# Optimization experiments

Measured on AMD Instinct MI355X. Metric: run time of the kernel, lower is better.

## Reference

```python
import math
import jax, jax.numpy as jnp
import numpy as np

D_MODEL = 1024
NUM_HEADS = 16
HEAD_DIM = D_MODEL // NUM_HEADS
EPS = 1e-8


def setup_inputs() -> dict:
    key = jax.random.key(0)
    ks = jax.random.split(key, 9)
    B, T = 2, 2048
    scale = 1.0 / math.sqrt(D_MODEL)
    return {
        "query": jax.random.normal(ks[0], (B, T, D_MODEL), jnp.float32),
        "key": jax.random.normal(ks[1], (B, T, D_MODEL), jnp.float32),
        "value": jax.random.normal(ks[2], (B, T, D_MODEL), jnp.float32),
        "key_padding_mask": jnp.zeros((B, T), dtype=bool),
        "Wq": jax.random.normal(ks[3], (D_MODEL, D_MODEL), jnp.float32) * scale,
        "Wk": jax.random.normal(ks[4], (D_MODEL, D_MODEL), jnp.float32) * scale,
        "Wv": jax.random.normal(ks[5], (D_MODEL, D_MODEL), jnp.float32) * scale,
        "Wo": jax.random.normal(ks[6], (D_MODEL, D_MODEL), jnp.float32) * scale,
        "s_v": jnp.zeros((NUM_HEADS,), jnp.float32),
        "s_r": jnp.zeros((NUM_HEADS,), jnp.float32),
    }


def _l2norm(x, eps=EPS):
    n = jnp.sqrt(jnp.sum(x * x, axis=-1, keepdims=True))
    return x / jnp.maximum(n, eps)


def _tanh_norm(x, eps=EPS):
    # Reconstructed TanhNorm: bound each head vector by tanh of its L2 norm.
    n = jnp.sqrt(jnp.sum(x * x, axis=-1, keepdims=True))
    return jnp.tanh(n) * x / (n + eps)


def reference(query, key, value, key_padding_mask, Wq, Wk, Wv, Wo, s_v, s_r):
    B, T_q, _ = query.shape
    T_k = key.shape[1]
    H, D = NUM_HEADS, HEAD_DIM

    def proj_split(x, W):  # torch Linear: x @ W.T, then split heads -> (B,H,T,D)
        y = jnp.einsum('btm,dm->btd', x, W)
        return y.reshape(x.shape[0], x.shape[1], H, D).transpose(0, 2, 1, 3)

    q = _l2norm(proj_split(query, Wq))
    k = _l2norm(proj_split(key, Wk))
    v = _l2norm(proj_split(value, Wv))

    sim = jnp.einsum('bhqd,bhkd->bhqk', q, k)  # cosine similarities

    w = jnp.exp(s_v) + 1.0  # (H,) window size per head
    r = jnp.exp(s_r) + 1.0  # (H,) sharpness per head

    # Trim-and-Square: alpha = relu(1 - r*(1 - sim))^2
    alpha = jax.nn.relu(1.0 - r[None, :, None, None] * (1.0 - sim)) ** 2

    # Causal cosine softmask: (H, T_q, T_k)
    rel = (jnp.arange(T_k)[None, :] - jnp.arange(T_q)[:, None]).astype(jnp.float32)
    w_ = w[:, None, None]
    cos_mask = 0.5 * (jnp.cos(jnp.pi * rel[None] / w_) + 1.0)
    in_window = (rel[None] > -w_) & (rel[None] <= 0)
    softmask = cos_mask * in_window.astype(jnp.float32)
    alpha = alpha * softmask[None]

    alpha = jnp.where(key_padding_mask[:, None, None, :], 0.0, alpha)

    out = jnp.einsum('bhqk,bhkd->bhqd', alpha, v)
    out = _tanh_norm(out)
    out = out.transpose(0, 2, 1, 3).reshape(B, T_q, H * D)
    return jnp.einsum('btm,dm->btd', out, Wo)
```

## Files before the change

kernel.cpp:

```cpp
#include <hip/hip_runtime.h>
#include <math.h>

#define D_MODEL 1024
#define NUM_HEADS 16
#define HEAD_DIM 64
#define EPS 1e-8f
#define B_SZ 2
#define T_SZ 2048
#define KEXP 2048

typedef unsigned short ushort_t;
typedef __attribute__((ext_vector_type(8))) short bf16x8;
typedef __attribute__((ext_vector_type(4))) float f32x4;

__device__ __forceinline__ ushort_t f2bf(float f) {
    unsigned u = __float_as_uint(f);
    unsigned r = (u + 0x7FFFu + ((u >> 16) & 1u)) >> 16;
    return (ushort_t)r;
}
__device__ __forceinline__ float bf2f(ushort_t h) {
    return __uint_as_float(((unsigned)h) << 16);
}

__device__ __forceinline__ void gload_lds16(const ushort_t* g, ushort_t* l) {
    __builtin_amdgcn_global_load_lds(
        (const __attribute__((address_space(1))) unsigned int*)g,
        (__attribute__((address_space(3))) unsigned int*)l, 16, 0, 0);
}

__global__ __launch_bounds__(256) void expand7(
    const float* q, const float* k, const float* v,
    const float* wq, const float* wk, const float* wv, const float* wo,
    ushort_t* qe, ushort_t* ke, ushort_t* ve,
    ushort_t* wqe, ushort_t* wke, ushort_t* wve, ushort_t* woe)
{
    const float* in; ushort_t* out; int rows;
    switch (blockIdx.z) {
        case 0: in = q;  out = qe;  rows = 4096; break;
        case 1: in = k;  out = ke;  rows = 4096; break;
        case 2: in = v;  out = ve;  rows = 4096; break;
        case 3: in = wq; out = wqe; rows = 1024; break;
        case 4: in = wk; out = wke; rows = 1024; break;
        case 5: in = wv; out = wve; rows = 1024; break;
        default: in = wo; out = woe; rows = 1024; break;
    }
    const int gid = blockIdx.x * 256 + threadIdx.x;
    const int total = rows * 1024;
    for (int e = gid * 8; e < total; e += 1024 * 256 * 8) {
        const int row = e >> 10;
        const int kk = e & 1023;

        float x[8];
        *(float4*)&x[0] = *(const float4*)&in[(size_t)row * 1024 + kk];
        *(float4*)&x[4] = *(const float4*)&in[(size_t)row * 1024 + kk + 4];

        union { ushort_t s[8]; uint4 u; } hi, lo;
        #pragma unroll
        for (int i = 0; i < 8; ++i) {
            ushort_t h = f2bf(x[i]);
            hi.s[i] = h;
            lo.s[i] = f2bf(x[i] - bf2f(h));
        }
        ushort_t* dst = out + (size_t)row * KEXP + (kk >> 5) * 64 + (kk & 31);
        *(uint4*)dst        = hi.u;
        *(uint4*)(dst + 32) = lo.u;
    }
}

__global__ __launch_bounds__(256) void gemm_sb3(
    const ushort_t* A0, const ushort_t* B0, float* C0,
    const ushort_t* A1, const ushort_t* B1, float* C1,
    const ushort_t* A2, const ushort_t* B2, float* C2,
    int M, int N)
{
    constexpr int BM = 128, BN = 128, WAVES_N = 2;
    constexpr int WAVE_M = 64, WAVE_N = 64, FM = 4, FN = 4;

    const int gx = gridDim.x, gy = gridDim.y;
    const int nwg = gx * gy * gridDim.z;
    const int lid = blockIdx.x + gx * (blockIdx.y + gy * blockIdx.z);
    const int cpx = nwg >> 3;
    const int swz = (lid & 7) * cpx + (lid >> 3);
    const int bz  = swz / (gx * gy);
    const int rem = swz - bz * gx * gy;
    const int by  = rem / gx;
    const int bx  = rem - by * gx;

    const ushort_t* Ae; const ushort_t* Be; float* C;
    if (bz == 0)      { Ae = A0; Be = B0; C = C0; }
    else if (bz == 1) { Ae = A1; Be = B1; C = C1; }
    else              { Ae = A2; Be = B2; C = C2; }

    __shared__ __align__(16) ushort_t As[BM * 64];
    __shared__ __align__(16) ushort_t Bs[BN * 64];

    const int tid = threadIdx.x;
    const int bm = by * BM;
    const int bn = bx * BN;

    const int rr = tid >> 3;
    const int p  = tid & 7;

    const int wid  = tid >> 6;
    const int wm   = wid / WAVES_N;
    const int wn   = wid % WAVES_N;
    const int lane = tid & 63;
    const int lrow = lane & 15;
    const int lk   = lane >> 4;

    f32x4 acc[FM][FN] = {};

    for (int ks = 0; ks < 32; ++ks) {
        const int kb = ks * 64;
        #pragma unroll
        for (int r = 0; r < 4; ++r) {
            const int row = r * 32 + rr;
            const int s = p ^ (row & 7);
            gload_lds16(Ae + (size_t)(bm + row) * KEXP + kb + s * 8,
                        &As[row * 64 + p * 8]);
        }
        #pragma unroll
        for (int r = 0; r < 4; ++r) {
            const int row = r * 32 + rr;
            const int s = p ^ (row & 7);
            gload_lds16(Be + (size_t)(bn + row) * KEXP + kb + s * 8,
                        &Bs[row * 64 + p * 8]);
        }
        __syncthreads();

        bf16x8 ah[FM], al[FM], bh[FN], bl[FN];
        #pragma unroll
        for (int m = 0; m < FM; ++m) {
            const int row = wm * WAVE_M + m * 16 + lrow;
            const int x = row & 7;
            ah[m] = *(const bf16x8*)&As[row * 64 + ((lk)     ^ x) * 8];
            al[m] = *(const bf16x8*)&As[row * 64 + ((lk + 4) ^ x) * 8];
        }
        #pragma unroll
        for (int n = 0; n < FN; ++n) {
            const int row = wn * WAVE_N + n * 16 + lrow;
            const int x = row & 7;
            bh[n] = *(const bf16x8*)&Bs[row * 64 + ((lk)     ^ x) * 8];
            bl[n] = *(const bf16x8*)&Bs[row * 64 + ((lk + 4) ^ x) * 8];
        }
        #pragma unroll
        for (int m = 0; m < FM; ++m)
            #pragma unroll
            for (int n = 0; n < FN; ++n) {
                acc[m][n] = __builtin_amdgcn_mfma_f32_16x16x32_bf16(ah[m], bh[n], acc[m][n], 0, 0, 0);
                acc[m][n] = __builtin_amdgcn_mfma_f32_16x16x32_bf16(al[m], bh[n], acc[m][n], 0, 0, 0);
                acc[m][n] = __builtin_amdgcn_mfma_f32_16x16x32_bf16(ah[m], bl[n], acc[m][n], 0, 0, 0);
            }
        __syncthreads();
    }

    #pragma unroll
    for (int m = 0; m < FM; ++m)
        #pragma unroll
        for (int j = 0; j < 4; ++j) {
            const int row = bm + wm * WAVE_M + m * 16 + lk * 4 + j;
            float* cr = C + (size_t)row * N + bn + wn * WAVE_N + lrow;
            #pragma unroll
            for (int n = 0; n < FN; ++n)
                cr[n * 16] = acc[m][n][j];
        }
}

template<int BN, int WAVES_M, int WAVES_N>
__global__ __launch_bounds__(256) void gemm_db(
    const ushort_t* A0, const ushort_t* B0, float* C0, int M, int N)
{
    constexpr int BM = 128;
    constexpr int WAVE_M = BM / WAVES_M;
    constexpr int WAVE_N = BN / WAVES_N;
    constexpr int FM = WAVE_M / 16;
    constexpr int FN = WAVE_N / 16;
    constexpr int NLD = BM / 32 + BN / 32;

    const int gx = gridDim.x;
    const int nwg = gx * gridDim.y;
    const int lid = blockIdx.x + gx * blockIdx.y;
    const int cpx = nwg >> 3;
    const int swz = (lid & 7) * cpx + (lid >> 3);
    const int by  = swz / gx;
    const int bx  = swz - by * gx;

    const ushort_t* Ae = A0; const ushort_t* Be = B0; float* C = C0;

    __shared__ __align__(16) ushort_t As0[BM * 64];
    __shared__ __align__(16) ushort_t As1[BM * 64];
    __shared__ __align__(16) ushort_t Bs0[BN * 64];
    __shared__ __align__(16) ushort_t Bs1[BN * 64];

    const int tid = threadIdx.x;
    const int bm = by * BM;
    const int bn = bx * BN;

    const int rr = tid >> 3;
    const int p  = tid & 7;

    const int wid  = tid >> 6;
    const int wm   = wid / WAVES_N;
    const int wn   = wid % WAVES_N;
    const int lane = tid & 63;
    const int lrow = lane & 15;
    const int lk   = lane >> 4;

    f32x4 acc[FM][FN] = {};

    auto stage = [&](ushort_t* AsP, ushort_t* BsP, int ks) {
        const int kb = ks * 64;
        #pragma unroll
        for (int r = 0; r < BM / 32; ++r) {
            const int row = r * 32 + rr;
            const int s = p ^ (row & 7);
            gload_lds16(Ae + (size_t)(bm + row) * KEXP + kb + s * 8,
                        &AsP[row * 64 + p * 8]);
        }
        #pragma unroll
        for (int r = 0; r < BN / 32; ++r) {
            const int row = r * 32 + rr;
            const int s = p ^ (row & 7);
            gload_lds16(Be + (size_t)(bn + row) * KEXP + kb + s * 8,
                        &BsP[row * 64 + p * 8]);
        }
    };

    auto compute = [&](const ushort_t* AsP, const ushort_t* BsP) {
        bf16x8 ah[FM], al[FM], bh[FN], bl[FN];
        #pragma unroll
        for (int m = 0; m < FM; ++m) {
            const int row = wm * WAVE_M + m * 16 + lrow;
            const int x = row & 7;
            ah[m] = *(const bf16x8*)&AsP[row * 64 + ((lk)     ^ x) * 8];
            al[m] = *(const bf16x8*)&AsP[row * 64 + ((lk + 4) ^ x) * 8];
        }
        #pragma unroll
        for (int n = 0; n < FN; ++n) {
            const int row = wn * WAVE_N + n * 16 + lrow;
            const int x = row & 7;
            bh[n] = *(const bf16x8*)&BsP[row * 64 + ((lk)     ^ x) * 8];
            bl[n] = *(const bf16x8*)&BsP[row * 64 + ((lk + 4) ^ x) * 8];
        }
        #pragma unroll
        for (int m = 0; m < FM; ++m)
            #pragma unroll
            for (int n = 0; n < FN; ++n) {
                acc[m][n] = __builtin_amdgcn_mfma_f32_16x16x32_bf16(ah[m], bh[n], acc[m][n], 0, 0, 0);
                acc[m][n] = __builtin_amdgcn_mfma_f32_16x16x32_bf16(al[m], bh[n], acc[m][n], 0, 0, 0);
                acc[m][n] = __builtin_amdgcn_mfma_f32_16x16x32_bf16(ah[m], bl[n], acc[m][n], 0, 0, 0);
            }
    };

    auto wait_nld = [&]() {
        if constexpr (NLD == 8)      asm volatile("s_waitcnt vmcnt(8)" ::: "memory");
        else if constexpr (NLD == 6) asm volatile("s_waitcnt vmcnt(6)" ::: "memory");
        else                         asm volatile("s_waitcnt vmcnt(0)" ::: "memory");
    };

    stage(As0, Bs0, 0);

    #pragma unroll 1
    for (int ks = 0; ks < 30; ks += 2) {
        stage(As1, Bs1, ks + 1);
        wait_nld();
        __builtin_amdgcn_s_barrier();
        __builtin_amdgcn_sched_barrier(0);
        compute(As0, Bs0);
        __builtin_amdgcn_s_barrier();

        stage(As0, Bs0, ks + 2);
        wait_nld();
        __builtin_amdgcn_s_barrier();
        __builtin_amdgcn_sched_barrier(0);
        compute(As1, Bs1);
        __builtin_amdgcn_s_barrier();
    }
    stage(As1, Bs1, 31);
    wait_nld();
    __builtin_amdgcn_s_barrier();
    __builtin_amdgcn_sched_barrier(0);
    compute(As0, Bs0);
    __builtin_amdgcn_s_barrier();

    asm volatile("s_waitcnt vmcnt(0)" ::: "memory");
    __builtin_amdgcn_s_barrier();
    __builtin_amdgcn_sched_barrier(0);
    compute(As1, Bs1);

    #pragma unroll
    for (int m = 0; m < FM; ++m)
        #pragma unroll
        for (int j = 0; j < 4; ++j) {
            const int row = bm + wm * WAVE_M + m * 16 + lk * 4 + j;
            float* cr = C + (size_t)row * N + bn + wn * WAVE_N + lrow;
            #pragma unroll
            for (int n = 0; n < FN; ++n)
                cr[n * 16] = acc[m][n][j];
        }
}

__device__ __forceinline__ float wred(float x) {
    #pragma unroll
    for (int off = 32; off; off >>= 1) x += __shfl_xor(x, off);
    return x;
}
__device__ __forceinline__ float frcp(float x) { return __builtin_amdgcn_rcpf(x); }

__global__ __launch_bounds__(256) void attn_kernel(
    const float* __restrict__ Q, const float* __restrict__ Kp, const float* __restrict__ Vp,
    const int* __restrict__ mask, const float* __restrict__ s_v, const float* __restrict__ s_r,
    ushort_t* __restrict__ Oe)
{
    const int lane = threadIdx.x & 63;
    const int wq = (blockIdx.x * blockDim.x + threadIdx.x) >> 6;
    const int i = wq % T_SZ;
    const int h = (wq / T_SZ) % NUM_HEADS;
    const int b = wq / (T_SZ * NUM_HEADS);

    const float w = __expf(s_v[h]) + 1.0f;
    const float r = __expf(s_r[h]) + 1.0f;
    const float inv_w = frcp(w);

    const size_t base = (size_t)(b * T_SZ) * D_MODEL + h * HEAD_DIM + lane;

    const float qv = Q[base + (size_t)i * D_MODEL];
    const float qn = qv * frcp(fmaxf(sqrtf(wred(qv * qv)), EPS));

    int jmin = i - (int)ceilf(w) + 1;
    if (jmin < 0) jmin = 0;

    float acc = 0.0f;
    for (int j = jmin; j <= i; ++j) {
        const float rel = (float)(j - i);
        if (!(rel > -w)) continue;
        const float kv = Kp[base + (size_t)j * D_MODEL];
        const float kn = kv * frcp(fmaxf(sqrtf(wred(kv * kv)), EPS));
        const float sim = wred(qn * kn);
        const float cm = 0.5f * (__cosf((float)M_PI * rel * inv_w) + 1.0f);
        const float a1 = fmaxf(1.0f - r * (1.0f - sim), 0.0f);
        float alpha = a1 * a1 * cm;
        if (mask[b * T_SZ + j] != 0) alpha = 0.0f;
        const float vv = Vp[base + (size_t)j * D_MODEL];
        const float vn = vv * frcp(fmaxf(sqrtf(wred(vv * vv)), EPS));
        acc += alpha * vn;
    }

    const float n = sqrtf(wred(acc * acc));
    const float th = 1.0f - 2.0f * frcp(__expf(2.0f * n) + 1.0f);
    const float o = th * acc * frcp(n + EPS);

    const int row = b * T_SZ + i;
    const int kg  = h * HEAD_DIM + lane;
    ushort_t hi = f2bf(o);
    ushort_t lo = f2bf(o - bf2f(hi));
    ushort_t* dst = Oe + (size_t)row * KEXP + (kg >> 5) * 64 + (kg & 31);
    dst[0]  = hi;
    dst[32] = lo;
}

extern "C" void kernel_launch(void* const* d_in, const int* in_sizes, int n_in,
                              void* d_out, int out_size, void* d_ws, size_t ws_size,
                              hipStream_t stream) {
    const float* query = (const float*)d_in[0];
    const float* key   = (const float*)d_in[1];
    const float* value = (const float*)d_in[2];
    const int*   mask  = (const int*)d_in[3];
    const float* Wq    = (const float*)d_in[4];
    const float* Wk    = (const float*)d_in[5];
    const float* Wv    = (const float*)d_in[6];
    const float* Wo    = (const float*)d_in[7];
    const float* s_v   = (const float*)d_in[8];
    const float* s_r   = (const float*)d_in[9];
    float* out = (float*)d_out;

    const int M = B_SZ * T_SZ;
    const size_t MB = 1u << 20;

    char* ws = (char*)d_ws;
    ushort_t* qe  = (ushort_t*)(ws + 0 * MB);
    ushort_t* ke  = (ushort_t*)(ws + 16 * MB);
    ushort_t* ve  = (ushort_t*)(ws + 32 * MB);
    ushort_t* wqe = (ushort_t*)(ws + 48 * MB);
    ushort_t* wke = (ushort_t*)(ws + 52 * MB);
    ushort_t* wve = (ushort_t*)(ws + 56 * MB);
    ushort_t* woe = (ushort_t*)(ws + 60 * MB);
    float*    qp  = (float*)(ws + 64 * MB);
    float*    kp  = (float*)(ws + 80 * MB);
    float*    vp  = (float*)(ws + 96 * MB);
    ushort_t* aoe = qe;

    hipLaunchKernelGGL(expand7, dim3(1024, 1, 7), dim3(256), 0, stream,
                       query, key, value, Wq, Wk, Wv, Wo,
                       qe, ke, ve, wqe, wke, wve, woe);

    hipLaunchKernelGGL(gemm_sb3, dim3(D_MODEL / 128, M / 128, 3), dim3(256), 0, stream,
                       qe, wqe, qp,
                       ke, wke, kp,
                       ve, wve, vp,
                       M, D_MODEL);

    const int total_waves = B_SZ * NUM_HEADS * T_SZ;
    hipLaunchKernelGGL(attn_kernel, dim3(total_waves / 4), dim3(256), 0, stream,
                       qp, kp, vp, mask, s_v, s_r, aoe);

    hipLaunchKernelGGL((gemm_db<64, 4, 1>), dim3(D_MODEL / 64, M / 128, 1), dim3(256), 0, stream,
                       aoe, woe, out, M, D_MODEL);
}
```

Baseline: 159.2 us.

## Map each attention query to one thread instead of one wavefront

Restructures the windowed attention kernel so each thread handles a full query head vector, computing norms and dot products serially with float4 loads. This removes the cross-lane shuffle reductions per key and vectorises the output stores. In exchange it gives strided, uncoalesced row loads across threads, far fewer waves in flight, and higher register use for the 64-element accumulator.

Measured after the change: 158.9 us, median of 2. About the same (-0.2%).

```diff
diff --git a/kernel.cpp b/kernel.cpp
--- a/kernel.cpp
+++ b/kernel.cpp
@@ -21,6 +21,7 @@
 __device__ __forceinline__ float bf2f(ushort_t h) {
     return __uint_as_float(((unsigned)h) << 16);
 }
+__device__ __forceinline__ float frcp(float x) { return __builtin_amdgcn_rcpf(x); }
 
 __device__ __forceinline__ void gload_lds16(const ushort_t* g, ushort_t* l) {
     __builtin_amdgcn_global_load_lds(
@@ -300,63 +301,100 @@
         }
 }
 
-__device__ __forceinline__ float wred(float x) {
-    #pragma unroll
-    for (int off = 32; off; off >>= 1) x += __shfl_xor(x, off);
-    return x;
-}
-__device__ __forceinline__ float frcp(float x) { return __builtin_amdgcn_rcpf(x); }
-
 __global__ __launch_bounds__(256) void attn_kernel(
     const float* __restrict__ Q, const float* __restrict__ Kp, const float* __restrict__ Vp,
     const int* __restrict__ mask, const float* __restrict__ s_v, const float* __restrict__ s_r,
     ushort_t* __restrict__ Oe)
 {
-    const int lane = threadIdx.x & 63;
-    const int wq = (blockIdx.x * blockDim.x + threadIdx.x) >> 6;
-    const int i = wq % T_SZ;
-    const int h = (wq / T_SZ) % NUM_HEADS;
-    const int b = wq / (T_SZ * NUM_HEADS);
+    const int gid = blockIdx.x * 256 + threadIdx.x;
+    const int i = gid % T_SZ;
+    const int h = (gid / T_SZ) % NUM_HEADS;
+    const int b = gid / (T_SZ * NUM_HEADS);
 
     const float w = __expf(s_v[h]) + 1.0f;
     const float r = __expf(s_r[h]) + 1.0f;
     const float inv_w = frcp(w);
 
-    const size_t base = (size_t)(b * T_SZ) * D_MODEL + h * HEAD_DIM + lane;
-
-    const float qv = Q[base + (size_t)i * D_MODEL];
-    const float qn = qv * frcp(fmaxf(sqrtf(wred(qv * qv)), EPS));
+    const size_t rowbase = (size_t)(b * T_SZ) * D_MODEL + h * HEAD_DIM;
+    const float4* qrow = (const float4*)(Q + rowbase + (size_t)i * D_MODEL);
+
+    float qq = 0.0f;
+    #pragma unroll
+    for (int g = 0; g < 16; ++g) {
+        float4 q4 = qrow[g];
+        qq = fmaf(q4.x, q4.x, fmaf(q4.y, q4.y, fmaf(q4.z, q4.z, fmaf(q4.w, q4.w, qq))));
+    }
+    const float qinv = frcp(fmaxf(sqrtf(qq), EPS));
 
     int jmin = i - (int)ceilf(w) + 1;
     if (jmin < 0) jmin = 0;
 
-    float acc = 0.0f;
+    float4 o[16];
+    #pragma unroll
+    for (int g = 0; g < 16; ++g) o[g] = make_float4(0.f, 0.f, 0.f, 0.f);
+
     for (int j = jmin; j <= i; ++j) {
         const float rel = (float)(j - i);
         if (!(rel > -w)) continue;
-        const float kv = Kp[base + (size_t)j * D_MODEL];
-        const float kn = kv * frcp(fmaxf(sqrtf(wred(kv * kv)), EPS));
-        const float sim = wred(qn * kn);
+        const float4* krow = (const float4*)(Kp + rowbase + (size_t)j * D_MODEL);
+        const float4* vrow = (const float4*)(Vp + rowbase + (size_t)j * D_MODEL);
+
+        float kk = 0.0f, qk = 0.0f, vv = 0.0f;
+        #pragma unroll
+        for (int g = 0; g < 16; ++g) {
+            float4 k4 = krow[g];
+            float4 q4 = qrow[g];
+            float4 v4 = vrow[g];
+            kk = fmaf(k4.x, k4.x, fmaf(k4.y, k4.y, fmaf(k4.z, k4.z, fmaf(k4.w, k4.w, kk))));
+            qk = fmaf(q4.x, k4.x, fmaf(q4.y, k4.y, fmaf(q4.z, k4.z, fmaf(q4.w, k4.w, qk))));
+            vv = fmaf(v4.x, v4.x, fmaf(v4.y, v4.y, fmaf(v4.z, v4.z, fmaf(v4.w, v4.w, vv))));
+        }
+        const float kinv = frcp(fmaxf(sqrtf(kk), EPS));
+        const float vinv = frcp(fmaxf(sqrtf(vv), EPS));
+        const float sim = qk * qinv * kinv;
+
         const float cm = 0.5f * (__cosf((float)M_PI * rel * inv_w) + 1.0f);
         const float a1 = fmaxf(1.0f - r * (1.0f - sim), 0.0f);
         float alpha = a1 * a1 * cm;
         if (mask[b * T_SZ + j] != 0) alpha = 0.0f;
-        const float vv = Vp[base + (size_t)j * D_MODEL];
-        const float vn = vv * frcp(fmaxf(sqrtf(wred(vv * vv)), EPS));
-        acc += alpha * vn;
-    }
-
-    const float n = sqrtf(wred(acc * acc));
+        const float av = alpha * vinv;
+
+        #pragma unroll
+        for (int g = 0; g < 16; ++g) {
+            float4 v4 = vrow[g];
+            o[g].x = fmaf(av, v4.x, o[g].x);
+            o[g].y = fmaf(av, v4.y, o[g].y);
+            o[g].z = fmaf(av, v4.z, o[g].z);
+            o[g].w = fmaf(av, v4.w, o[g].w);
+        }
+    }
+
+    float oo = 0.0f;
+    #pragma unroll
+    for (int g = 0; g < 16; ++g)
+        oo = fmaf(o[g].x, o[g].x, fmaf(o[g].y, o[g].y, fmaf(o[g].z, o[g].z, fmaf(o[g].w, o[g].w, oo))));
+    const float n = sqrtf(oo);
     const float th = 1.0f - 2.0f * frcp(__expf(2.0f * n) + 1.0f);
-    const float o = th * acc * frcp(n + EPS);
+    const float sc = th * frcp(n + EPS);
 
     const int row = b * T_SZ + i;
-    const int kg  = h * HEAD_DIM + lane;
-    ushort_t hi = f2bf(o);
-    ushort_t lo = f2bf(o - bf2f(hi));
-    ushort_t* dst = Oe + (size_t)row * KEXP + (kg >> 5) * 64 + (kg & 31);
-    dst[0]  = hi;
-    dst[32] = lo;
+    ushort_t* orow = Oe + (size_t)row * KEXP;
+    #pragma unroll
+    for (int g = 0; g < 16; ++g) {
+        const int kg = h * HEAD_DIM + g * 4;
+        ushort_t* dst = orow + (kg >> 5) * 64 + (kg & 31);
+        float x0 = o[g].x * sc, x1 = o[g].y * sc, x2 = o[g].z * sc, x3 = o[g].w * sc;
+        ushort_t h0 = f2bf(x0), h1 = f2bf(x1), h2 = f2bf(x2), h3 = f2bf(x3);
+        ushort_t l0 = f2bf(x0 - bf2f(h0)), l1 = f2bf(x1 - bf2f(h1));
+        ushort_t l2 = f2bf(x2 - bf2f(h2)), l3 = f2bf(x3 - bf2f(h3));
+        uint2 hw, lw;
+        hw.x = (unsigned)h0 | ((unsigned)h1 << 16);
+        hw.y = (unsigned)h2 | ((unsigned)h3 << 16);
+        lw.x = (unsigned)l0 | ((unsigned)l1 << 16);
+        lw.y = (unsigned)l2 | ((unsigned)l3 << 16);
+        *(uint2*)dst        = hw;
+        *(uint2*)(dst + 32) = lw;
+    }
 }
 
 extern "C" void kernel_launch(void* const* d_in, const int* in_sizes, int n_in,
@@ -400,8 +438,8 @@
                        ve, wve, vp,
                        M, D_MODEL);
 
-    const int total_waves = B_SZ * NUM_HEADS * T_SZ;
-    hipLaunchKernelGGL(attn_kernel, dim3(total_waves / 4), dim3(256), 0, stream,
+    const int total_threads = B_SZ * NUM_HEADS * T_SZ;
+    hipLaunchKernelGGL(attn_kernel, dim3(total_threads / 256), dim3(256), 0, stream,
                        qp, kp, vp, mask, s_v, s_r, aoe);
 
     hipLaunchKernelGGL((gemm_db<64, 4, 1>), dim3(D_MODEL / 64, M / 128, 1), dim3(256), 0, stream,
```
